# Kernel optimization log

Measured on AMD Instinct MI355X. Metric: run time of the kernel, lower is better.

## Reference

```python
import jax, jax.numpy as jnp
import numpy as np

N, E, D = 50000, 600000, 128

def _lin(key, fan_in, fan_out):
    kw, kb = jax.random.split(key)
    s = 1.0 / np.sqrt(fan_in)
    W = jax.random.uniform(kw, (fan_in, fan_out), minval=-s, maxval=s, dtype=jnp.float32)
    b = jax.random.uniform(kb, (fan_out,), minval=-s, maxval=s, dtype=jnp.float32)
    return W, b

def setup_inputs() -> dict:
    key = jax.random.key(0)
    ks = jax.random.split(key, 16)
    h = jax.random.normal(ks[0], (N, D), dtype=jnp.float32)
    pos = jax.random.normal(ks[1], (N, 2), dtype=jnp.float32)
    edge_index = jax.random.randint(ks[2], (2, E), 0, N, dtype=jnp.int64)
    edge_attr = jax.random.uniform(ks[3], (E, 1), dtype=jnp.float32)
    Wq, bq = _lin(ks[4], D, D)
    Wk, bk = _lin(ks[5], D, D)
    Wv, bv = _lin(ks[6], D, D)
    We1, be1 = _lin(ks[7], 1, D)
    We2, be2 = _lin(ks[8], D, D)
    Wa1, ba1 = _lin(ks[9], 3 * D, D)
    Wa2, ba2 = _lin(ks[10], D, 1)
    Wm1, bm1 = _lin(ks[11], 2 * D, D)
    Wm2, bm2 = _lin(ks[12], D, D)
    return dict(h=h, pos=pos, edge_index=edge_index, edge_attr=edge_attr,
                Wq=Wq, bq=bq, Wk=Wk, bk=bk, Wv=Wv, bv=bv,
                We1=We1, be1=be1, We2=We2, be2=be2,
                Wa1=Wa1, ba1=ba1, Wa2=Wa2, ba2=ba2,
                Wm1=Wm1, bm1=bm1, Wm2=Wm2, bm2=bm2)

def reference(h, pos, edge_index, edge_attr,
              Wq, bq, Wk, bk, Wv, bv,
              We1, be1, We2, be2,
              Wa1, ba1, Wa2, ba2,
              Wm1, bm1, Wm2, bm2):
    row, col = edge_index[0], edge_index[1]  # source, destination
    q = h @ Wq + bq                          # [N, D]
    k = h @ Wk + bk
    v = h @ Wv + bv
    e = jax.nn.relu(edge_attr @ We1 + be1) @ We2 + be2  # [E, D]
    # per-edge attention logits
    attn_in = jnp.concatenate([q[col], k[row], e], axis=-1)          # [E, 3D]
    logits = (jax.nn.relu(attn_in @ Wa1 + ba1) @ Wa2 + ba2)[:, 0]    # [E]
    # segment softmax grouped by destination node (torch_geometric style)
    seg_max = jax.ops.segment_max(logits, col, num_segments=N)       # [N]
    ex = jnp.exp(logits - seg_max[col])
    seg_sum = jax.ops.segment_sum(ex, col, num_segments=N)           # [N]
    w = ex / (seg_sum[col] + 1e-16)                                  # [E]
    # per-edge messages
    msg_in = jnp.concatenate([v[row], e], axis=-1)                   # [E, 2D]
    msg = jax.nn.silu(msg_in @ Wm1 + bm1) @ Wm2 + bm2                # [E, D]
    agg = jax.ops.segment_sum(msg * w[:, None], col, num_segments=N) # [N, D]
    return (h + agg, pos)
```

## Files before the change

kernel.cpp:

```cpp
#include <hip/hip_runtime.h>
#include <math.h>

#define D 128
#define SB 256

typedef __attribute__((ext_vector_type(8))) short bf16x8;
typedef __attribute__((ext_vector_type(4))) float f32x4;

__device__ inline unsigned f2bf(float f) {
    unsigned u = __float_as_uint(f);
    return (u + 0x7FFFu + ((u >> 16) & 1u)) >> 16;
}

__global__ __launch_bounds__(128) void prep(
    const float* __restrict__ Wq, const float* __restrict__ bq,
    const float* __restrict__ Wk, const float* __restrict__ bk,
    const float* __restrict__ Wv, const float* __restrict__ bv,
    const float* __restrict__ Wa1, const float* __restrict__ ba1,
    const float* __restrict__ Wm1, const float* __restrict__ bm1,
    const float* __restrict__ We1, const float* __restrict__ be1,
    const float* __restrict__ We2, const float* __restrict__ be2,
    const float* __restrict__ Wm2,
    const int* __restrict__ ei, int E,
    ushort* __restrict__ Wpk, ushort* __restrict__ Wpk2,
    float* __restrict__ bqa, float* __restrict__ bka, float* __restrict__ bva,
    float* __restrict__ bounds,
    float2* __restrict__ AB, float2* __restrict__ MB,
    int* __restrict__ deg)
{
    int b = blockIdx.x;
    int j = threadIdx.x;
    if (b < 384) {
        int which = b >> 7, i = b & 127;
        const float *A, *B;
        if (which == 0)      { A = Wq; B = Wa1; }
        else if (which == 1) { A = Wk; B = Wa1 + 128 * D; }
        else                 { A = Wv; B = Wm1; }
        float acc = 0.f;
        for (int k = 0; k < D; k++) acc += A[i * D + k] * B[k * D + j];
        int gc = which * 128 + j;
        int nt = gc >> 4;
        int ks = i >> 5;
        int lane = (((i >> 3) & 3) << 4) | (gc & 15);
        int j8 = i & 7;
        Wpk[((nt * 4 + ks) * 64 + lane) * 8 + j8] = (ushort)f2bf(acc);
    } else if (b < 387) {
        int which = b - 384;
        const float *bias, *B, *extra; float *out;
        if (which == 0)      { bias = bq; B = Wa1;           out = bqa; extra = ba1; }
        else if (which == 1) { bias = bk; B = Wa1 + 128 * D; out = bka; extra = nullptr; }
        else                 { bias = bv; B = Wm1;           out = bva; extra = bm1; }
        float acc = extra ? extra[j] : 0.f;
        for (int k = 0; k < D; k++) acc += bias[k] * B[k * D + j];
        out[j] = acc;
    } else if (b == 387) {
        __shared__ float sb[128];
        float w = We1[j], bb = be1[j];
        float t = (w != 0.f) ? (-bb / w) : 2.f;
        t = fminf(fmaxf(t, 0.f), 1.f);
        sb[j] = t;
        __syncthreads();
        for (int k = 2; k <= 128; k <<= 1)
            for (int jj = k >> 1; jj > 0; jj >>= 1) {
                int ixj = j ^ jj;
                if (ixj > j) {
                    float a = sb[j], c = sb[ixj];
                    bool up = ((j & k) == 0);
                    if (up ? (a > c) : (a < c)) { sb[j] = c; sb[ixj] = a; }
                }
                __syncthreads();
            }
        if (j == 0) { bounds[0] = 0.f; bounds[129] = 1.f; }
        bounds[1 + j] = sb[j];
    } else if (b < 517) {
        __shared__ float sb[128];
        __shared__ float Ae[128], Be[128];
        float w = We1[j], bb = be1[j];
        float t = (w != 0.f) ? (-bb / w) : 2.f;
        t = fminf(fmaxf(t, 0.f), 1.f);
        sb[j] = t;
        __syncthreads();
        for (int k = 2; k <= 128; k <<= 1)
            for (int jj = k >> 1; jj > 0; jj >>= 1) {
                int ixj = j ^ jj;
                if (ixj > j) {
                    float a = sb[j], c = sb[ixj];
                    bool up = ((j & k) == 0);
                    if (up ? (a > c) : (a < c)) { sb[j] = c; sb[ixj] = a; }
                }
                __syncthreads();
            }
        int i = b - 388;
        float lo = (i == 0)   ? 0.f : sb[i - 1];
        float hi = (i == 128) ? 1.f : sb[i];
        float m = 0.5f * (lo + hi);
        float ae = 0.f, be = 0.f;
        for (int k = 0; k < 128; k++) {
            float ww = We1[k], bb2 = be1[k];
            if (m * ww + bb2 > 0.f) { ae += ww * We2[k * D + j]; be += bb2 * We2[k * D + j]; }
        }
        be += be2[j];
        Ae[j] = ae; Be[j] = be;
        __syncthreads();
        float aa = 0.f, ba = 0.f, am = 0.f, bm = 0.f;
        for (int l = 0; l < 128; l++) {
            float ael = Ae[l], bel = Be[l];
            float wa = Wa1[(256 + l) * D + j];
            float wm = Wm1[(128 + l) * D + j];
            aa += ael * wa; ba += bel * wa;
            am += ael * wm; bm += bel * wm;
        }
        AB[i * 128 + j] = make_float2(aa, ba);
        MB[i * 128 + j] = make_float2(am, bm);
    } else if (b < 645) {
        int i = b - 517;
        int nt = j >> 4;
        int ks = i >> 5;
        int lane = (((i >> 3) & 3) << 4) | (j & 15);
        int j8 = i & 7;
        Wpk2[((nt * 4 + ks) * 64 + lane) * 8 + j8] = (ushort)f2bf(Wm2[i * D + j]);
    } else {
        int e = (b - 645) * 128 + j;
        if (e < E) atomicAdd(deg + ei[E + e], 1);
    }
}

__global__ __launch_bounds__(SB) void k_scan1(const int* __restrict__ deg, int N,
                                              int* __restrict__ partial)
{
    __shared__ int ls[SB];
    int t = threadIdx.x;
    int i = blockIdx.x * SB + t;
    ls[t] = (i < N) ? deg[i] : 0;
    __syncthreads();
    for (int s = SB / 2; s > 0; s >>= 1) {
        if (t < s) ls[t] += ls[t + s];
        __syncthreads();
    }
    if (t == 0) partial[blockIdx.x] = ls[0];
}

__global__ __launch_bounds__(SB) void k_scan23(const int* __restrict__ deg, int N,
                                               const int* __restrict__ partial, int NB,
                                               int* __restrict__ off)
{
    __shared__ int lp[SB];
    __shared__ int ls[SB];
    int t = threadIdx.x;
    int pv = (t < NB) ? partial[t] : 0;
    lp[t] = pv;
    __syncthreads();
    int pval = pv;
    for (int s = 1; s < SB; s <<= 1) {
        int add = (t >= s) ? lp[t - s] : 0;
        __syncthreads();
        pval += add;
        lp[t] = pval;
        __syncthreads();
    }
    int base = (blockIdx.x > 0) ? lp[blockIdx.x - 1] : 0;

    int i = blockIdx.x * SB + t;
    int v = (i < N) ? deg[i] : 0;
    ls[t] = v;
    __syncthreads();
    int val = v;
    for (int s = 1; s < SB; s <<= 1) {
        int add = (t >= s) ? ls[t - s] : 0;
        __syncthreads();
        val += add;
        ls[t] = val;
        __syncthreads();
    }
    if (i < N) off[i] = base + val - v;
}

__global__ __launch_bounds__(256) void k_scatter(const int* __restrict__ ei,
                                                 const float* __restrict__ eattr, int E,
                                                 const float* __restrict__ bounds,
                                                 int* __restrict__ off, int2* __restrict__ recs)
{
    __shared__ float bnd[130];
    int t = threadIdx.x;
    if (t < 130) bnd[t] = bounds[t];
    __syncthreads();
    int e = blockIdx.x * 256 + t;
    if (e >= E) return;
    int row = ei[e], col = ei[E + e];
    float a = eattr[e];
    int lo = 0, hi = 128;
    while (lo < hi) { int mid = (lo + hi + 1) >> 1; if (bnd[mid] <= a) lo = mid; else hi = mid - 1; }
    int p = atomicAdd(off + col, 1);
    recs[p] = make_int2(row | (lo << 17), __float_as_int(a));
}

__global__ __launch_bounds__(256) void node_gemm(
    const float* __restrict__ h, int N,
    const ushort* __restrict__ Wpk,
    const float* __restrict__ bqa, const float* __restrict__ bka, const float* __restrict__ bva,
    float* __restrict__ qa, unsigned* __restrict__ kv)
{
    __shared__ __align__(16) ushort hsb[64 * 128];
    int t = threadIdx.x;
    int row0 = blockIdx.x * 64;
#pragma unroll
    for (int i = 0; i < 4; i++) {
        int g = t + i * 256;
        int r = g >> 4, c = g & 15;
        int grow = row0 + r;
        float4 f0, f1;
        if (grow < N) {
            const float4* hp = (const float4*)(h + (size_t)grow * D + c * 8);
            f0 = hp[0]; f1 = hp[1];
        } else {
            f0 = make_float4(0.f, 0.f, 0.f, 0.f); f1 = f0;
        }
        ushort u[8] = { (ushort)f2bf(f0.x), (ushort)f2bf(f0.y), (ushort)f2bf(f0.z), (ushort)f2bf(f0.w),
                        (ushort)f2bf(f1.x), (ushort)f2bf(f1.y), (ushort)f2bf(f1.z), (ushort)f2bf(f1.w) };
        int pc = c ^ (r & 15);
        *(uint4*)&hsb[r * 128 + pc * 8] = *(uint4*)u;
    }
    __syncthreads();

    int w = t >> 6, l = t & 63;
    int lrow = w * 16 + (l & 15);
    f32x4 acc[24];
#pragma unroll
    for (int i = 0; i < 24; i++) acc[i] = (f32x4){0.f, 0.f, 0.f, 0.f};

    const bf16x8* WB = (const bf16x8*)Wpk;
#pragma unroll
    for (int ks = 0; ks < 4; ks++) {
        int c = (ks * 4 + (l >> 4)) ^ (l & 15);
        bf16x8 afrag = *(const bf16x8*)&hsb[lrow * 128 + c * 8];
#pragma unroll
        for (int nt = 0; nt < 24; nt++) {
            bf16x8 bfrag = WB[(nt * 4 + ks) * 64 + l];
            acc[nt] = __builtin_amdgcn_mfma_f32_16x16x32_bf16(afrag, bfrag, acc[nt], 0, 0, 0);
        }
    }

    int rbase = row0 + w * 16 + ((l >> 4) << 2);
    int cl = l & 15;
#pragma unroll
    for (int cc = 0; cc < 8; cc++) {
        float bqv = bqa[cc * 16 + cl];
        float bkv = bka[cc * 16 + cl];
        float bvv = bva[cc * 16 + cl];
        f32x4 aq = acc[cc], ak = acc[8 + cc], av = acc[16 + cc];
#pragma unroll
        for (int r = 0; r < 4; r++) {
            int row = rbase + r;
            if (row < N) {
                qa[(size_t)row * D + cc * 16 + cl] = aq[r] + bqv;
                kv[(size_t)row * D + cc * 16 + cl] =
                    (f2bf(av[r] + bvv) << 16) | f2bf(ak[r] + bkv);
            }
        }
    }
}

__global__ __launch_bounds__(256) void node_all(
    const int2* __restrict__ recs, int N,
    const int* __restrict__ off,
    const float* __restrict__ qa, const unsigned* __restrict__ kv,
    const float2* __restrict__ AB, const float2* __restrict__ MB,
    const float* __restrict__ Wa2,
    unsigned* __restrict__ Sb, float* __restrict__ segsum)
{
    int t = threadIdx.x;
    int l = t & 31;
    int n = blockIdx.x * 8 + (t >> 5);
    bool valid = (n < N);
    int start = 0, end = 0;
    if (valid) {
        end = off[n];
        start = (n > 0) ? off[n - 1] : 0;
    }

    const char* kvc = (const char*)kv;
    const char* ABc = (const char*)AB;
    const char* MBc = (const char*)MB;

    float4 q4 = valid ? *(const float4*)(qa + (size_t)n * D + 4 * l)
                      : make_float4(0.f, 0.f, 0.f, 0.f);
    float4 w4 = *(const float4*)(Wa2 + 4 * l);

    float m_run = -INFINITY;
    float a0 = 0.f, a1 = 0.f, a2 = 0.f, a3 = 0.f, ssum = 0.f;

    int idx = start;
    for (; idx + 2 <= end; idx += 2) {
        int2 rec1 = recs[idx];
        int2 rec2 = recs[idx + 1];
        unsigned u1 = (unsigned)rec1.x, u2 = (unsigned)rec2.x;
        float at1 = __int_as_float(rec1.y), at2 = __int_as_float(rec2.y);
        int rb1 = (int)(u1 & 0x1FFFFu) << 9, tb1 = (int)(u1 >> 17) << 10;
        int rb2 = (int)(u2 & 0x1FFFFu) << 9, tb2 = (int)(u2 >> 17) << 10;

        uint4 kp1 = *(const uint4*)(kvc + rb1 + (l << 4));
        uint4 kp2 = *(const uint4*)(kvc + rb2 + (l << 4));
        float4 ab0a = *(const float4*)(ABc + tb1 + (l << 5));
        float4 ab1a = *(const float4*)(ABc + tb1 + (l << 5) + 16);
        float4 mb0a = *(const float4*)(MBc + tb1 + (l << 5));
        float4 mb1a = *(const float4*)(MBc + tb1 + (l << 5) + 16);
        float4 ab0b = *(const float4*)(ABc + tb2 + (l << 5));
        float4 ab1b = *(const float4*)(ABc + tb2 + (l << 5) + 16);
        float4 mb0b = *(const float4*)(MBc + tb2 + (l << 5));
        float4 mb1b = *(const float4*)(MBc + tb2 + (l << 5) + 16);

        float p1 = fmaxf(q4.x + __uint_as_float(kp1.x << 16) + at1 * ab0a.x + ab0a.y, 0.f) * w4.x
                 + fmaxf(q4.y + __uint_as_float(kp1.y << 16) + at1 * ab0a.z + ab0a.w, 0.f) * w4.y
                 + fmaxf(q4.z + __uint_as_float(kp1.z << 16) + at1 * ab1a.x + ab1a.y, 0.f) * w4.z
                 + fmaxf(q4.w + __uint_as_float(kp1.w << 16) + at1 * ab1a.z + ab1a.w, 0.f) * w4.w;
        float p2 = fmaxf(q4.x + __uint_as_float(kp2.x << 16) + at2 * ab0b.x + ab0b.y, 0.f) * w4.x
                 + fmaxf(q4.y + __uint_as_float(kp2.y << 16) + at2 * ab0b.z + ab0b.w, 0.f) * w4.y
                 + fmaxf(q4.z + __uint_as_float(kp2.z << 16) + at2 * ab1b.x + ab1b.y, 0.f) * w4.z
                 + fmaxf(q4.w + __uint_as_float(kp2.w << 16) + at2 * ab1b.z + ab1b.w, 0.f) * w4.w;
#pragma unroll
        for (int s = 1; s < 32; s <<= 1) {
            p1 += __shfl_xor(p1, s, 64);
            p2 += __shfl_xor(p2, s, 64);
        }
        float d1 = p1 - m_run, d2 = p2 - m_run;
        if (fmaxf(d1, d2) > 8.f) {
            float mN = fmaxf(fmaxf(p1, p2), m_run);
            float sc = __expf(m_run - mN);
            a0 *= sc; a1 *= sc; a2 *= sc; a3 *= sc; ssum *= sc;
            m_run = mN; d1 = p1 - mN; d2 = p2 - mN;
        }
        float ex1 = __expf(d1), ex2 = __expf(d2);

        float x0 = __uint_as_float(kp1.x & 0xFFFF0000u) + at1 * mb0a.x + mb0a.y;
        float x1 = __uint_as_float(kp1.y & 0xFFFF0000u) + at1 * mb0a.z + mb0a.w;
        float x2 = __uint_as_float(kp1.z & 0xFFFF0000u) + at1 * mb1a.x + mb1a.y;
        float x3 = __uint_as_float(kp1.w & 0xFFFF0000u) + at1 * mb1a.z + mb1a.w;
        float y0 = __uint_as_float(kp2.x & 0xFFFF0000u) + at2 * mb0b.x + mb0b.y;
        float y1 = __uint_as_float(kp2.y & 0xFFFF0000u) + at2 * mb0b.z + mb0b.w;
        float y2 = __uint_as_float(kp2.z & 0xFFFF0000u) + at2 * mb1b.x + mb1b.y;
        float y3 = __uint_as_float(kp2.w & 0xFFFF0000u) + at2 * mb1b.z + mb1b.w;
        float s10 = x0 * __builtin_amdgcn_rcpf(1.f + __expf(-x0));
        float s11 = x1 * __builtin_amdgcn_rcpf(1.f + __expf(-x1));
        float s12 = x2 * __builtin_amdgcn_rcpf(1.f + __expf(-x2));
        float s13 = x3 * __builtin_amdgcn_rcpf(1.f + __expf(-x3));
        float s20 = y0 * __builtin_amdgcn_rcpf(1.f + __expf(-y0));
        float s21 = y1 * __builtin_amdgcn_rcpf(1.f + __expf(-y1));
        float s22 = y2 * __builtin_amdgcn_rcpf(1.f + __expf(-y2));
        float s23 = y3 * __builtin_amdgcn_rcpf(1.f + __expf(-y3));

        a0 = fmaf(ex2, s20, fmaf(ex1, s10, a0));
        a1 = fmaf(ex2, s21, fmaf(ex1, s11, a1));
        a2 = fmaf(ex2, s22, fmaf(ex1, s12, a2));
        a3 = fmaf(ex2, s23, fmaf(ex1, s13, a3));
        ssum += ex1 + ex2;
    }
    if (idx < end) {
        int2 rec = recs[idx];
        unsigned u1 = (unsigned)rec.x;
        float a = __int_as_float(rec.y);
        int rb = (int)(u1 & 0x1FFFFu) << 9, tb = (int)(u1 >> 17) << 10;
        uint4 kp = *(const uint4*)(kvc + rb + (l << 4));
        float4 ab0 = *(const float4*)(ABc + tb + (l << 5));
        float4 ab1 = *(const float4*)(ABc + tb + (l << 5) + 16);
        float4 mb0 = *(const float4*)(MBc + tb + (l << 5));
        float4 mb1 = *(const float4*)(MBc + tb + (l << 5) + 16);
        float p1 = fmaxf(q4.x + __uint_as_float(kp.x << 16) + a * ab0.x + ab0.y, 0.f) * w4.x
                 + fmaxf(q4.y + __uint_as_float(kp.y << 16) + a * ab0.z + ab0.w, 0.f) * w4.y
                 + fmaxf(q4.z + __uint_as_float(kp.z << 16) + a * ab1.x + ab1.y, 0.f) * w4.z
                 + fmaxf(q4.w + __uint_as_float(kp.w << 16) + a * ab1.z + ab1.w, 0.f) * w4.w;
#pragma unroll
        for (int s = 1; s < 32; s <<= 1) p1 += __shfl_xor(p1, s, 64);
        float d1 = p1 - m_run;
        if (d1 > 8.f) {
            float mN = p1;
            float sc = __expf(m_run - mN);
            a0 *= sc; a1 *= sc; a2 *= sc; a3 *= sc; ssum *= sc;
            m_run = mN; d1 = 0.f;
        }
        float ex = __expf(d1);
        float x0 = __uint_as_float(kp.x & 0xFFFF0000u) + a * mb0.x + mb0.y;
        float x1 = __uint_as_float(kp.y & 0xFFFF0000u) + a * mb0.z + mb0.w;
        float x2 = __uint_as_float(kp.z & 0xFFFF0000u) + a * mb1.x + mb1.y;
        float x3 = __uint_as_float(kp.w & 0xFFFF0000u) + a * mb1.z + mb1.w;
        a0 = fmaf(ex, x0 * __builtin_amdgcn_rcpf(1.f + __expf(-x0)), a0);
        a1 = fmaf(ex, x1 * __builtin_amdgcn_rcpf(1.f + __expf(-x1)), a1);
        a2 = fmaf(ex, x2 * __builtin_amdgcn_rcpf(1.f + __expf(-x2)), a2);
        a3 = fmaf(ex, x3 * __builtin_amdgcn_rcpf(1.f + __expf(-x3)), a3);
        ssum += ex;
    }

    if (valid) {
        float inv = __builtin_amdgcn_rcpf(ssum + 1e-16f);
        unsigned pw0 = f2bf(a0 * inv) | (f2bf(a1 * inv) << 16);
        unsigned pw1 = f2bf(a2 * inv) | (f2bf(a3 * inv) << 16);
        *(uint2*)(Sb + (size_t)n * 64 + 2 * l) = make_uint2(pw0, pw1);
        if (l == 0) segsum[n] = ssum;
    }
}

__global__ __launch_bounds__(256) void node_out(
    const float* __restrict__ h, int N,
    const unsigned* __restrict__ Sb, const ushort* __restrict__ Wpk2,
    const float* __restrict__ bm2, const float* __restrict__ segsum,
    float* __restrict__ out, const float* __restrict__ pos, int npos, int G1)
{
    int b = blockIdx.x;
    int t = threadIdx.x;
    if (b >= G1) {
        int i = ((b - G1) * 256 + t) * 4;
        float* outp = out + (size_t)N * D;
        if (i + 3 < npos) {
            *(float4*)(outp + i) = *(const float4*)(pos + i);
        } else {
            for (int j = i; j < npos; j++) outp[j] = pos[j];
        }
        return;
    }
    __shared__ __align__(16) ushort ssb[64 * 128];
    int row0 = b * 64;
#pragma unroll
    for (int i = 0; i < 4; i++) {
        int g = t + i * 256;
        int r = g >> 4, c = g & 15;
        int grow = row0 + r;
        uint4 u = make_uint4(0u, 0u, 0u, 0u);
        if (grow < N) u = *(const uint4*)(Sb + (size_t)grow * 64 + c * 4);
        int pc = c ^ (r & 15);
        *(uint4*)&ssb[r * 128 + pc * 8] = u;
    }
    __syncthreads();

    int w = t >> 6, l = t & 63;
    int lrow = w * 16 + (l & 15);
    f32x4 acc[8];
#pragma unroll
    for (int i = 0; i < 8; i++) acc[i] = (f32x4){0.f, 0.f, 0.f, 0.f};

    const bf16x8* WB = (const bf16x8*)Wpk2;
#pragma unroll
    for (int ks = 0; ks < 4; ks++) {
        int c = (ks * 4 + (l >> 4)) ^ (l & 15);
        bf16x8 afrag = *(const bf16x8*)&ssb[lrow * 128 + c * 8];
#pragma unroll
        for (int nt = 0; nt < 8; nt++) {
            bf16x8 bfrag = WB[(nt * 4 + ks) * 64 + l];
            acc[nt] = __builtin_amdgcn_mfma_f32_16x16x32_bf16(afrag, bfrag, acc[nt], 0, 0, 0);
        }
    }

    int rbase = row0 + w * 16 + ((l >> 4) << 2);
    int cl = l & 15;
#pragma unroll
    for (int cc = 0; cc < 8; cc++) {
        float bb = bm2[cc * 16 + cl];
        f32x4 av = acc[cc];
#pragma unroll
        for (int r = 0; r < 4; r++) {
            int row = rbase + r;
            if (row < N) {
                float ws_ = segsum[row];
                ws_ = ws_ / (ws_ + 1e-16f);
                out[(size_t)row * D + cc * 16 + cl] =
                    h[(size_t)row * D + cc * 16 + cl] + av[r] + bb * ws_;
            }
        }
    }
}

extern "C" void kernel_launch(void* const* d_in, const int* in_sizes, int n_in,
                              void* d_out, int out_size, void* d_ws, size_t ws_size,
                              hipStream_t stream)
{
    const float* h     = (const float*)d_in[0];
    const float* pos   = (const float*)d_in[1];
    const int*   ei    = (const int*)d_in[2];
    const float* eattr = (const float*)d_in[3];
    const float* Wq  = (const float*)d_in[4];  const float* bq  = (const float*)d_in[5];
    const float* Wk  = (const float*)d_in[6];  const float* bk  = (const float*)d_in[7];
    const float* Wv  = (const float*)d_in[8];  const float* bv  = (const float*)d_in[9];
    const float* We1 = (const float*)d_in[10]; const float* be1 = (const float*)d_in[11];
    const float* We2 = (const float*)d_in[12]; const float* be2 = (const float*)d_in[13];
    const float* Wa1 = (const float*)d_in[14]; const float* ba1 = (const float*)d_in[15];
    const float* Wa2 = (const float*)d_in[16];
    const float* Wm1 = (const float*)d_in[18]; const float* bm1 = (const float*)d_in[19];
    const float* Wm2 = (const float*)d_in[20]; const float* bm2 = (const float*)d_in[21];

    int N = in_sizes[0] / D;
    int E = in_sizes[3];
    int NB = (N + SB - 1) / SB;

    float* ws = (float*)d_ws;
    size_t off_f = 0;
    auto alloc = [&](size_t n) { float* p = ws + off_f; off_f += (n + 63) & ~(size_t)63; return p; };

    ushort* Wpk  = (ushort*)alloc(24 * 4 * 64 * 8 / 2);
    ushort* Wpk2 = (ushort*)alloc(8 * 4 * 64 * 8 / 2);
    float* bqa = alloc(D); float* bka = alloc(D); float* bva = alloc(D);
    float* bounds = alloc(130);
    float2* AB = (float2*)alloc((size_t)129 * 128 * 2);
    float2* MB = (float2*)alloc((size_t)129 * 128 * 2);
    float* qa = alloc((size_t)N * D);
    unsigned* kv = (unsigned*)alloc((size_t)N * D);
    unsigned* Sb = (unsigned*)alloc((size_t)N * 64);
    float* segsum = alloc(N);
    int* deg  = (int*)alloc(N);
    int* offs = (int*)alloc(N);
    int* partial = (int*)alloc(256);
    int2* recs = (int2*)alloc((size_t)E * 2);

    hipMemsetAsync(deg, 0, (size_t)N * 4, stream);

    int HB = (E + 127) / 128;
    prep<<<645 + HB, 128, 0, stream>>>(Wq, bq, Wk, bk, Wv, bv, Wa1, ba1, Wm1, bm1,
                                       We1, be1, We2, be2, Wm2, ei, E,
                                       Wpk, Wpk2, bqa, bka, bva, bounds, AB, MB, deg);

    k_scan1<<<NB, SB, 0, stream>>>(deg, N, partial);
    k_scan23<<<NB, SB, 0, stream>>>(deg, N, partial, NB, offs);

    node_gemm<<<(N + 63) / 64, 256, 0, stream>>>(h, N, Wpk, bqa, bka, bva, qa, kv);

    k_scatter<<<(E + 255) / 256, 256, 0, stream>>>(ei, eattr, E, bounds, offs, recs);

    node_all<<<(N + 7) / 8, 256, 0, stream>>>(recs, N, offs, qa, kv, AB, MB, Wa2,
                                              Sb, segsum);

    int G1 = (N + 63) / 64;
    int G2 = (2 * N + 1023) / 1024;
    node_out<<<G1 + G2, 256, 0, stream>>>(h, N, Sb, Wpk2, bm2, segsum, (float*)d_out,
                                          pos, 2 * N, G1);
}
```

Before: 251.3 us.

## Split node edge loop across two half-waves, store q in bf16, widen prep blocks

```diff
diff --git a/kernel.cpp b/kernel.cpp
--- a/kernel.cpp
+++ b/kernel.cpp
@@ -12,7 +12,7 @@
     return (u + 0x7FFFu + ((u >> 16) & 1u)) >> 16;
 }
 
-__global__ __launch_bounds__(128) void prep(
+__global__ __launch_bounds__(256) void prep(
     const float* __restrict__ Wq, const float* __restrict__ bq,
     const float* __restrict__ Wk, const float* __restrict__ bk,
     const float* __restrict__ Wv, const float* __restrict__ bv,
@@ -28,8 +28,10 @@
     float2* __restrict__ AB, float2* __restrict__ MB,
     int* __restrict__ deg)
 {
+    __shared__ float smem[1536];
     int b = blockIdx.x;
-    int j = threadIdx.x;
+    int t = threadIdx.x;
+    int j = t & 127, half = t >> 7;
     if (b < 384) {
         int which = b >> 7, i = b & 127;
         const float *A, *B;
@@ -37,56 +39,71 @@
         else if (which == 1) { A = Wk; B = Wa1 + 128 * D; }
         else                 { A = Wv; B = Wm1; }
         float acc = 0.f;
-        for (int k = 0; k < D; k++) acc += A[i * D + k] * B[k * D + j];
-        int gc = which * 128 + j;
-        int nt = gc >> 4;
-        int ks = i >> 5;
-        int lane = (((i >> 3) & 3) << 4) | (gc & 15);
-        int j8 = i & 7;
-        Wpk[((nt * 4 + ks) * 64 + lane) * 8 + j8] = (ushort)f2bf(acc);
+        for (int k = half * 64; k < half * 64 + 64; k++) acc += A[i * D + k] * B[k * D + j];
+        smem[t] = acc;
+        __syncthreads();
+        if (half == 0) {
+            float v = smem[j] + smem[128 + j];
+            int gc = which * 128 + j;
+            int nt = gc >> 4;
+            int ks = i >> 5;
+            int lane = (((i >> 3) & 3) << 4) | (gc & 15);
+            int j8 = i & 7;
+            Wpk[((nt * 4 + ks) * 64 + lane) * 8 + j8] = (ushort)f2bf(v);
+        }
     } else if (b < 387) {
         int which = b - 384;
         const float *bias, *B, *extra; float *out;
         if (which == 0)      { bias = bq; B = Wa1;           out = bqa; extra = ba1; }
         else if (which == 1) { bias = bk; B = Wa1 + 128 * D; out = bka; extra = nullptr; }
         else                 { bias = bv; B = Wm1;           out = bva; extra = bm1; }
-        float acc = extra ? extra[j] : 0.f;
-        for (int k = 0; k < D; k++) acc += bias[k] * B[k * D + j];
-        out[j] = acc;
+        float acc = 0.f;
+        for (int k = half * 64; k < half * 64 + 64; k++) acc += bias[k] * B[k * D + j];
+        smem[t] = acc;
+        __syncthreads();
+        if (half == 0) out[j] = smem[j] + smem[128 + j] + (extra ? extra[j] : 0.f);
     } else if (b == 387) {
-        __shared__ float sb[128];
-        float w = We1[j], bb = be1[j];
-        float t = (w != 0.f) ? (-bb / w) : 2.f;
-        t = fminf(fmaxf(t, 0.f), 1.f);
-        sb[j] = t;
+        float* sb = smem;
+        if (t < 128) {
+            float w = We1[t], bb = be1[t];
+            float th = (w != 0.f) ? (-bb / w) : 2.f;
+            sb[t] = fminf(fmaxf(th, 0.f), 1.f);
+        }
         __syncthreads();
         for (int k = 2; k <= 128; k <<= 1)
             for (int jj = k >> 1; jj > 0; jj >>= 1) {
-                int ixj = j ^ jj;
-                if (ixj > j) {
-                    float a = sb[j], c = sb[ixj];
-                    bool up = ((j & k) == 0);
-                    if (up ? (a > c) : (a < c)) { sb[j] = c; sb[ixj] = a; }
+                if (t < 128) {
+                    int ixj = t ^ jj;
+                    if (ixj > t) {
+                        float a = sb[t], c = sb[ixj];
+                        bool up = ((t & k) == 0);
+                        if (up ? (a > c) : (a < c)) { sb[t] = c; sb[ixj] = a; }
+                    }
                 }
                 __syncthreads();
             }
-        if (j == 0) { bounds[0] = 0.f; bounds[129] = 1.f; }
-        bounds[1 + j] = sb[j];
+        if (t == 0) { bounds[0] = 0.f; bounds[129] = 1.f; }
+        if (t < 128) bounds[1 + t] = sb[t];
     } else if (b < 517) {
-        __shared__ float sb[128];
-        __shared__ float Ae[128], Be[128];
-        float w = We1[j], bb = be1[j];
-        float t = (w != 0.f) ? (-bb / w) : 2.f;
-        t = fminf(fmaxf(t, 0.f), 1.f);
-        sb[j] = t;
+        float* sb = smem;
+        float* Ae = smem + 128;
+        float* Be = smem + 256;
+        float* P  = smem + 384;
+        if (t < 128) {
+            float w = We1[t], bb = be1[t];
+            float th = (w != 0.f) ? (-bb / w) : 2.f;
+            sb[t] = fminf(fmaxf(th, 0.f), 1.f);
+        }
         __syncthreads();
         for (int k = 2; k <= 128; k <<= 1)
             for (int jj = k >> 1; jj > 0; jj >>= 1) {
-                int ixj = j ^ jj;
-                if (ixj > j) {
-                    float a = sb[j], c = sb[ixj];
-                    bool up = ((j & k) == 0);
-                    if (up ? (a > c) : (a < c)) { sb[j] = c; sb[ixj] = a; }
+                if (t < 128) {
+                    int ixj = t ^ jj;
+                    if (ixj > t) {
+                        float a = sb[t], c = sb[ixj];
+                        bool up = ((t & k) == 0);
+                        if (up ? (a > c) : (a < c)) { sb[t] = c; sb[ixj] = a; }
+                    }
                 }
                 __syncthreads();
             }
@@ -95,32 +112,42 @@
         float hi = (i == 128) ? 1.f : sb[i];
         float m = 0.5f * (lo + hi);
         float ae = 0.f, be = 0.f;
-        for (int k = 0; k < 128; k++) {
+        for (int k = half * 64; k < half * 64 + 64; k++) {
             float ww = We1[k], bb2 = be1[k];
             if (m * ww + bb2 > 0.f) { ae += ww * We2[k * D + j]; be += bb2 * We2[k * D + j]; }
         }
-        be += be2[j];
-        Ae[j] = ae; Be[j] = be;
+        P[t] = ae; P[256 + t] = be;
+        __syncthreads();
+        if (half == 0) {
+            Ae[j] = P[j] + P[128 + j];
+            Be[j] = P[256 + j] + P[384 + j] + be2[j];
+        }
         __syncthreads();
         float aa = 0.f, ba = 0.f, am = 0.f, bm = 0.f;
-        for (int l = 0; l < 128; l++) {
-            float ael = Ae[l], bel = Be[l];
-            float wa = Wa1[(256 + l) * D + j];
-            float wm = Wm1[(128 + l) * D + j];
+        for (int l2 = half * 64; l2 < half * 64 + 64; l2++) {
+            float ael = Ae[l2], bel = Be[l2];
+            float wa = Wa1[(256 + l2) * D + j];
+            float wm = Wm1[(128 + l2) * D + j];
             aa += ael * wa; ba += bel * wa;
             am += ael * wm; bm += bel * wm;
         }
-        AB[i * 128 + j] = make_float2(aa, ba);
-        MB[i * 128 + j] = make_float2(am, bm);
+        P[t] = aa; P[256 + t] = ba; P[512 + t] = am; P[768 + t] = bm;
+        __syncthreads();
+        if (half == 0) {
+            AB[i * 128 + j] = make_float2(P[j] + P[128 + j], P[256 + j] + P[384 + j]);
+            MB[i * 128 + j] = make_float2(P[512 + j] + P[640 + j], P[768 + j] + P[896 + j]);
+        }
     } else if (b < 645) {
-        int i = b - 517;
-        int nt = j >> 4;
-        int ks = i >> 5;
-        int lane = (((i >> 3) & 3) << 4) | (j & 15);
-        int j8 = i & 7;
-        Wpk2[((nt * 4 + ks) * 64 + lane) * 8 + j8] = (ushort)f2bf(Wm2[i * D + j]);
+        if (t < 128) {
+            int i = b - 517;
+            int nt = t >> 4;
+            int ks = i >> 5;
+            int lane = (((i >> 3) & 3) << 4) | (t & 15);
+            int j8 = i & 7;
+            Wpk2[((nt * 4 + ks) * 64 + lane) * 8 + j8] = (ushort)f2bf(Wm2[i * D + t]);
+        }
     } else {
-        int e = (b - 645) * 128 + j;
+        int e = (b - 645) * 256 + t;
         if (e < E) atomicAdd(deg + ei[E + e], 1);
     }
 }
@@ -198,7 +225,7 @@
     const float* __restrict__ h, int N,
     const ushort* __restrict__ Wpk,
     const float* __restrict__ bqa, const float* __restrict__ bka, const float* __restrict__ bva,
-    float* __restrict__ qa, unsigned* __restrict__ kv)
+    ushort* __restrict__ qb, unsigned* __restrict__ kv)
 {
     __shared__ __align__(16) ushort hsb[64 * 128];
     int t = threadIdx.x;
@@ -252,7 +279,7 @@
         for (int r = 0; r < 4; r++) {
             int row = rbase + r;
             if (row < N) {
-                qa[(size_t)row * D + cc * 16 + cl] = aq[r] + bqv;
+                qb[(size_t)row * D + cc * 16 + cl] = (ushort)f2bf(aq[r] + bqv);
                 kv[(size_t)row * D + cc * 16 + cl] =
                     (f2bf(av[r] + bvv) << 16) | f2bf(ak[r] + bkv);
             }
@@ -263,36 +290,40 @@
 __global__ __launch_bounds__(256) void node_all(
     const int2* __restrict__ recs, int N,
     const int* __restrict__ off,
-    const float* __restrict__ qa, const unsigned* __restrict__ kv,
+    const ushort* __restrict__ qb, const unsigned* __restrict__ kv,
     const float2* __restrict__ AB, const float2* __restrict__ MB,
     const float* __restrict__ Wa2,
     unsigned* __restrict__ Sb, float* __restrict__ segsum)
 {
     int t = threadIdx.x;
-    int l = t & 31;
-    int n = blockIdx.x * 8 + (t >> 5);
-    bool valid = (n < N);
-    int start = 0, end = 0;
-    if (valid) {
-        end = off[n];
-        start = (n > 0) ? off[n - 1] : 0;
-    }
+    int lane = t & 63;
+    int slot = lane >> 5;
+    int l = lane & 31;
+    int n = blockIdx.x * 4 + (t >> 6);
+    if (n >= N) return;
+    int end = off[n];
+    int start = (n > 0) ? off[n - 1] : 0;
 
     const char* kvc = (const char*)kv;
     const char* ABc = (const char*)AB;
     const char* MBc = (const char*)MB;
 
-    float4 q4 = valid ? *(const float4*)(qa + (size_t)n * D + 4 * l)
-                      : make_float4(0.f, 0.f, 0.f, 0.f);
+    uint2 qp = *(const uint2*)(qb + (size_t)n * D + 4 * l);
+    float q0 = __uint_as_float(qp.x << 16);
+    float q1 = __uint_as_float(qp.x & 0xFFFF0000u);
+    float q2 = __uint_as_float(qp.y << 16);
+    float q3 = __uint_as_float(qp.y & 0xFFFF0000u);
     float4 w4 = *(const float4*)(Wa2 + 4 * l);
 
     float m_run = -INFINITY;
     float a0 = 0.f, a1 = 0.f, a2 = 0.f, a3 = 0.f, ssum = 0.f;
 
-    int idx = start;
-    for (; idx + 2 <= end; idx += 2) {
-        int2 rec1 = recs[idx];
-        int2 rec2 = recs[idx + 1];
+    for (int idx = start; idx < end; idx += 4) {
+        int i1 = idx + slot;
+        int i2 = idx + 2 + slot;
+        bool lv1 = i1 < end, lv2 = i2 < end;
+        int2 rec1 = recs[lv1 ? i1 : start];
+        int2 rec2 = recs[lv2 ? i2 : start];
         unsigned u1 = (unsigned)rec1.x, u2 = (unsigned)rec2.x;
         float at1 = __int_as_float(rec1.y), at2 = __int_as_float(rec2.y);
         int rb1 = (int)(u1 & 0x1FFFFu) << 9, tb1 = (int)(u1 >> 17) << 10;
@@ -309,27 +340,31 @@
         float4 mb0b = *(const float4*)(MBc + tb2 + (l << 5));
         float4 mb1b = *(const float4*)(MBc + tb2 + (l << 5) + 16);
 
-        float p1 = fmaxf(q4.x + __uint_as_float(kp1.x << 16) + at1 * ab0a.x + ab0a.y, 0.f) * w4.x
-                 + fmaxf(q4.y + __uint_as_float(kp1.y << 16) + at1 * ab0a.z + ab0a.w, 0.f) * w4.y
-                 + fmaxf(q4.z + __uint_as_float(kp1.z << 16) + at1 * ab1a.x + ab1a.y, 0.f) * w4.z
-                 + fmaxf(q4.w + __uint_as_float(kp1.w << 16) + at1 * ab1a.z + ab1a.w, 0.f) * w4.w;
-        float p2 = fmaxf(q4.x + __uint_as_float(kp2.x << 16) + at2 * ab0b.x + ab0b.y, 0.f) * w4.x
-                 + fmaxf(q4.y + __uint_as_float(kp2.y << 16) + at2 * ab0b.z + ab0b.w, 0.f) * w4.y
-                 + fmaxf(q4.z + __uint_as_float(kp2.z << 16) + at2 * ab1b.x + ab1b.y, 0.f) * w4.z
-                 + fmaxf(q4.w + __uint_as_float(kp2.w << 16) + at2 * ab1b.z + ab1b.w, 0.f) * w4.w;
+        float p1 = fmaxf(q0 + __uint_as_float(kp1.x << 16) + at1 * ab0a.x + ab0a.y, 0.f) * w4.x
+                 + fmaxf(q1 + __uint_as_float(kp1.y << 16) + at1 * ab0a.z + ab0a.w, 0.f) * w4.y
+                 + fmaxf(q2 + __uint_as_float(kp1.z << 16) + at1 * ab1a.x + ab1a.y, 0.f) * w4.z
+                 + fmaxf(q3 + __uint_as_float(kp1.w << 16) + at1 * ab1a.z + ab1a.w, 0.f) * w4.w;
+        float p2 = fmaxf(q0 + __uint_as_float(kp2.x << 16) + at2 * ab0b.x + ab0b.y, 0.f) * w4.x
+                 + fmaxf(q1 + __uint_as_float(kp2.y << 16) + at2 * ab0b.z + ab0b.w, 0.f) * w4.y
+                 + fmaxf(q2 + __uint_as_float(kp2.z << 16) + at2 * ab1b.x + ab1b.y, 0.f) * w4.z
+                 + fmaxf(q3 + __uint_as_float(kp2.w << 16) + at2 * ab1b.z + ab1b.w, 0.f) * w4.w;
 #pragma unroll
         for (int s = 1; s < 32; s <<= 1) {
             p1 += __shfl_xor(p1, s, 64);
             p2 += __shfl_xor(p2, s, 64);
         }
-        float d1 = p1 - m_run, d2 = p2 - m_run;
-        if (fmaxf(d1, d2) > 8.f) {
-            float mN = fmaxf(fmaxf(p1, p2), m_run);
+        float pm1 = lv1 ? p1 : -INFINITY;
+        float pm2 = lv2 ? p2 : -INFINITY;
+        float pmx = fmaxf(pm1, pm2);
+        pmx = fmaxf(pmx, __shfl_xor(pmx, 32, 64));
+        if (pmx - m_run > 8.f) {
+            float mN = fmaxf(m_run, pmx);
             float sc = __expf(m_run - mN);
             a0 *= sc; a1 *= sc; a2 *= sc; a3 *= sc; ssum *= sc;
-            m_run = mN; d1 = p1 - mN; d2 = p2 - mN;
-        }
-        float ex1 = __expf(d1), ex2 = __expf(d2);
+            m_run = mN;
+        }
+        float ex1 = __expf(pm1 - m_run);
+        float ex2 = __expf(pm2 - m_run);
 
         float x0 = __uint_as_float(kp1.x & 0xFFFF0000u) + at1 * mb0a.x + mb0a.y;
         float x1 = __uint_as_float(kp1.y & 0xFFFF0000u) + at1 * mb0a.z + mb0a.w;
@@ -354,42 +389,14 @@
         a3 = fmaf(ex2, s23, fmaf(ex1, s13, a3));
         ssum += ex1 + ex2;
     }
-    if (idx < end) {
-        int2 rec = recs[idx];
-        unsigned u1 = (unsigned)rec.x;
-        float a = __int_as_float(rec.y);
-        int rb = (int)(u1 & 0x1FFFFu) << 9, tb = (int)(u1 >> 17) << 10;
-        uint4 kp = *(const uint4*)(kvc + rb + (l << 4));
-        float4 ab0 = *(const float4*)(ABc + tb + (l << 5));
-        float4 ab1 = *(const float4*)(ABc + tb + (l << 5) + 16);
-        float4 mb0 = *(const float4*)(MBc + tb + (l << 5));
-        float4 mb1 = *(const float4*)(MBc + tb + (l << 5) + 16);
-        float p1 = fmaxf(q4.x + __uint_as_float(kp.x << 16) + a * ab0.x + ab0.y, 0.f) * w4.x
-                 + fmaxf(q4.y + __uint_as_float(kp.y << 16) + a * ab0.z + ab0.w, 0.f) * w4.y
-                 + fmaxf(q4.z + __uint_as_float(kp.z << 16) + a * ab1.x + ab1.y, 0.f) * w4.z
-                 + fmaxf(q4.w + __uint_as_float(kp.w << 16) + a * ab1.z + ab1.w, 0.f) * w4.w;
-#pragma unroll
-        for (int s = 1; s < 32; s <<= 1) p1 += __shfl_xor(p1, s, 64);
-        float d1 = p1 - m_run;
-        if (d1 > 8.f) {
-            float mN = p1;
-            float sc = __expf(m_run - mN);
-            a0 *= sc; a1 *= sc; a2 *= sc; a3 *= sc; ssum *= sc;
-            m_run = mN; d1 = 0.f;
-        }
-        float ex = __expf(d1);
-        float x0 = __uint_as_float(kp.x & 0xFFFF0000u) + a * mb0.x + mb0.y;
-        float x1 = __uint_as_float(kp.y & 0xFFFF0000u) + a * mb0.z + mb0.w;
-        float x2 = __uint_as_float(kp.z & 0xFFFF0000u) + a * mb1.x + mb1.y;
-        float x3 = __uint_as_float(kp.w & 0xFFFF0000u) + a * mb1.z + mb1.w;
-        a0 = fmaf(ex, x0 * __builtin_amdgcn_rcpf(1.f + __expf(-x0)), a0);
-        a1 = fmaf(ex, x1 * __builtin_amdgcn_rcpf(1.f + __expf(-x1)), a1);
-        a2 = fmaf(ex, x2 * __builtin_amdgcn_rcpf(1.f + __expf(-x2)), a2);
-        a3 = fmaf(ex, x3 * __builtin_amdgcn_rcpf(1.f + __expf(-x3)), a3);
-        ssum += ex;
-    }
-
-    if (valid) {
+
+    a0 += __shfl_xor(a0, 32, 64);
+    a1 += __shfl_xor(a1, 32, 64);
+    a2 += __shfl_xor(a2, 32, 64);
+    a3 += __shfl_xor(a3, 32, 64);
+    ssum += __shfl_xor(ssum, 32, 64);
+
+    if (slot == 0) {
         float inv = __builtin_amdgcn_rcpf(ssum + 1e-16f);
         unsigned pw0 = f2bf(a0 * inv) | (f2bf(a1 * inv) << 16);
         unsigned pw1 = f2bf(a2 * inv) | (f2bf(a3 * inv) << 16);
@@ -499,7 +506,7 @@
     float* bounds = alloc(130);
     float2* AB = (float2*)alloc((size_t)129 * 128 * 2);
     float2* MB = (float2*)alloc((size_t)129 * 128 * 2);
-    float* qa = alloc((size_t)N * D);
+    ushort* qb = (ushort*)alloc((size_t)N * 64);
     unsigned* kv = (unsigned*)alloc((size_t)N * D);
     unsigned* Sb = (unsigned*)alloc((size_t)N * 64);
     float* segsum = alloc(N);
@@ -510,19 +517,19 @@
 
     hipMemsetAsync(deg, 0, (size_t)N * 4, stream);
 
-    int HB = (E + 127) / 128;
-    prep<<<645 + HB, 128, 0, stream>>>(Wq, bq, Wk, bk, Wv, bv, Wa1, ba1, Wm1, bm1,
+    int HB = (E + 255) / 256;
+    prep<<<645 + HB, 256, 0, stream>>>(Wq, bq, Wk, bk, Wv, bv, Wa1, ba1, Wm1, bm1,
                                        We1, be1, We2, be2, Wm2, ei, E,
                                        Wpk, Wpk2, bqa, bka, bva, bounds, AB, MB, deg);
 
     k_scan1<<<NB, SB, 0, stream>>>(deg, N, partial);
     k_scan23<<<NB, SB, 0, stream>>>(deg, N, partial, NB, offs);
 
-    node_gemm<<<(N + 63) / 64, 256, 0, stream>>>(h, N, Wpk, bqa, bka, bva, qa, kv);
+    node_gemm<<<(N + 63) / 64, 256, 0, stream>>>(h, N, Wpk, bqa, bka, bva, qb, kv);
 
     k_scatter<<<(E + 255) / 256, 256, 0, stream>>>(ei, eattr, E, bounds, offs, recs);
 
-    node_all<<<(N + 7) / 8, 256, 0, stream>>>(recs, N, offs, qa, kv, AB, MB, Wa2,
+    node_all<<<(N + 3) / 4, 256, 0, stream>>>(recs, N, offs, qb, kv, AB, MB, Wa2,
                                               Sb, segsum);
 
     int G1 = (N + 63) / 64;
```

Result: slower. 259.9 us (+3.4%).
